# Performance work log

Measured on AMD Instinct MI355X. Metric: run time of the kernel, lower is better.

Reference implementation:

```python
import jax, jax.numpy as jnp
import numpy as np

B, NCH, NPTS, NGT = 8, 4, 1024, 10
NANCH = 5 * NPTS
NMIN, NMAX = 64, 64
M = NMIN + NMAX
NPOOL = 64
EXT = 0.2
EPS = 1e-5
PERM = np.array([3, 4, 5, 1, 0, 2, 6])

_C = jnp.array([[0., 1, 0], [0, -1, 0], [2.5, -1, 0], [2.5, 1, 0], [2.5, 0, 0]], jnp.float32)
_ROT = jnp.array([[1., 0, 0], [0, 0, 1], [0, 1, 0]], jnp.float32)  # theta=0 rotation from source
NEW_CENTERS = _C @ _ROT  # (5,3)
DIM = jnp.array([2., 2., 5.], jnp.float32)


def _conv1x1(x, w, b):
    return jnp.einsum('bci,oc->boi', x, w) + b[None, :, None]


def _bn(x, g, be):  # BatchNorm1d in train mode: batch stats over (N, L)
    m = x.mean((0, 2), keepdims=True)
    v = ((x - m) ** 2).mean((0, 2), keepdims=True)
    return (x - m) * jax.lax.rsqrt(v + EPS) * g[None, :, None] + be[None, :, None]


def _corners(b):  # b=(cx,cz,w,l,ry) -> (4,2) CCW BEV corners
    lx = jnp.array([0.5, -0.5, -0.5, 0.5]) * b[2]
    lz = jnp.array([0.5, 0.5, -0.5, -0.5]) * b[3]
    c, s = jnp.cos(b[4]), jnp.sin(b[4])
    return jnp.stack([b[0] + lx * c - lz * s, b[1] + lx * s + lz * c], 1)


def _clip(poly, count, e1, e2):  # Sutherland-Hodgman: clip convex poly (8,2) by left half-plane of e1->e2
    idx = jnp.arange(8)
    valid = idx < count
    cnt = jnp.maximum(count, 1)
    nxt = poly[(idx + 1) % cnt]
    ex, ez = e2[0] - e1[0], e2[1] - e1[1]
    dc = ex * (poly[:, 1] - e1[1]) - ez * (poly[:, 0] - e1[0])
    dn = ex * (nxt[:, 1] - e1[1]) - ez * (nxt[:, 0] - e1[0])
    in_c, in_n = dc >= 0, dn >= 0
    den = dc - dn
    t = dc / jnp.where(jnp.abs(den) < 1e-9, 1e-9, den)
    inter = poly + t[:, None] * (nxt - poly)
    flags = jnp.stack([valid & in_c, valid & (in_c ^ in_n)], 1).reshape(16)
    pts = jnp.stack([poly, inter], 1).reshape(16, 2)
    pos = jnp.cumsum(flags) - 1
    out = jnp.zeros((8, 2), poly.dtype).at[jnp.where(flags, pos, 8)].set(pts, mode='drop')
    return out, flags.sum()


def _bev_iou(a, b):  # rotated BEV IoU, a,b=(cx,cz,w,l,ry)
    poly = jnp.zeros((8, 2)).at[:4].set(_corners(a))
    count = jnp.int32(4)
    cb = _corners(b)
    for k in range(4):
        poly, count = _clip(poly, count, cb[k], cb[(k + 1) % 4])
    idx = jnp.arange(8)
    nxt = poly[(idx + 1) % jnp.maximum(count, 1)]
    inter = 0.5 * jnp.abs(jnp.sum(jnp.where(idx < count, poly[:, 0] * nxt[:, 1] - nxt[:, 0] * poly[:, 1], 0.)))
    return inter / jnp.maximum(a[2] * a[3] + b[2] * b[3] - inter, 1e-8)


def _bev(b7):  # (..,7)=[x,y,z,h,w,l,ry] -> (cx,cz,w,l,ry)
    return jnp.stack([b7[..., 0], b7[..., 2], b7[..., 4], b7[..., 5], b7[..., 6]], -1)


def _select_one(pnts, labels):  # pnts (N,3), labels (G,9)
    cent = (pnts[:, None, :] - NEW_CENTERS[None]).reshape(NANCH, 3)  # repeat_interleave(pnts,5)-tile(centers)
    anchors = jnp.concatenate([jnp.broadcast_to(DIM, (NANCH, 3)), cent, jnp.zeros((NANCH, 1))], 1)
    a7 = anchors[:, PERM]
    g7 = labels[:, PERM]
    ab, gb = _bev(a7), _bev(g7)
    iou2d = jax.vmap(lambda g: jax.vmap(lambda a: _bev_iou(g, a))(ab))(gb)  # (G, NANCH)
    max_iou = iou2d.max(0)
    max_ind = jnp.argmax(iou2d, 0)
    order = jnp.argsort(max_iou)
    sel = jnp.concatenate([order[:NMIN], order[-NMAX:]])  # bottom-k + top-k
    return a7[sel], max_ind[sel], max_iou[sel]


def _pool_one(box, pts, ft):  # roipool3d: first NPOOL points inside expanded box, zero-padded
    c, s = jnp.cos(box[6]), jnp.sin(box[6])
    dx, dz = pts[:, 0] - box[0], pts[:, 2] - box[2]
    xl = dx * c + dz * s
    zl = -dx * s + dz * c
    inside = (jnp.abs(xl) < box[4] * 0.5 + EXT) & (jnp.abs(zl) < box[5] * 0.5 + EXT) \
             & (pts[:, 1] > box[1] - box[3] - EXT) & (pts[:, 1] < box[1] + EXT)
    order = jnp.argsort(jnp.logical_not(inside))[:NPOOL]  # stable sort: inside points first, original order
    valid = inside[order].astype(ft.dtype)[:, None]
    return jnp.concatenate([ft[order], pts[order]], -1) * valid  # (NPOOL, 256+3)


def _forward(points, gt_labels, p):
    x = jax.nn.relu(_bn(_conv1x1(points, p['pn_w1'], p['pn_b1']), p['pn_g1'], p['pn_be1']))
    x = jax.nn.relu(_bn(_conv1x1(x, p['pn_w2'], p['pn_b2']), p['pn_g2'], p['pn_be2']))
    x = _bn(_conv1x1(x, p['pn_w3'], p['pn_b3']), p['pn_g3'], p['pn_be3'])  # (B,256,N)
    pts = jnp.transpose(points[:, :3, :], (0, 2, 1))  # (B,N,3)
    sel_boxes, sel_idx, sel_iou = jax.vmap(_select_one)(pts, gt_labels)  # (B,M,7),(B,M),(B,M)
    ftr = jnp.transpose(x, (0, 2, 1))  # (B,N,256)
    pooled = jax.vmap(lambda bx, pp, ff: jax.vmap(lambda b: _pool_one(b, pp, ff))(bx))(sel_boxes, pts, ftr)
    pooled = pooled - jnp.pad(sel_boxes[:, :, None, :3], ((0, 0), (0, 0), (0, 0), (256, 0)))  # subtract center from last 3 ch
    pf = jnp.transpose(pooled.reshape(B * M, NPOOL, 259), (0, 2, 1))  # (B*M,259,64)
    f = _bn(_conv1x1(pf, p['rp_w1'], p['rp_b1']), p['rp_g1'], p['rp_be1'])
    f = _bn(_conv1x1(f, p['rp_w2'], p['rp_b2']), p['rp_g2'], p['rp_be2'])
    feats = f.reshape(B, M, 1024, NPOOL).max(-1)
    labels_bin = (sel_iou > 0.5).astype(jnp.int32)
    return feats, labels_bin, sel_iou, sel_boxes, gt_labels[-1], sel_idx


def setup_inputs():
    key = jax.random.key(0)
    ks = jax.random.split(key, 16)
    points = jax.random.normal(ks[0], (B, NCH, NPTS), jnp.float32) * 3.0
    dims = jax.random.uniform(ks[1], (B, NGT, 3), minval=1.0, maxval=4.0)
    ctrs = jax.random.normal(ks[2], (B, NGT, 3)) * 3.0
    th = jax.random.uniform(ks[3], (B, NGT, 1), minval=-3.14, maxval=3.14)
    extra = jax.random.normal(ks[4], (B, NGT, 2))
    gt_labels = jnp.concatenate([dims, ctrs, th, extra], -1).astype(jnp.float32)  # (B,G,9)
    inp = {'points': points, 'gt_labels': gt_labels}
    shapes = [('pn', 1, 64, NCH), ('pn', 2, 128, 64), ('pn', 3, 256, 128), ('rp', 1, 512, 259), ('rp', 2, 1024, 512)]
    for j, (pre, n, o, i) in enumerate(shapes):
        inp[f'{pre}_w{n}'] = jax.random.normal(ks[5 + j], (o, i), jnp.float32) / np.sqrt(i).astype(np.float32)
        inp[f'{pre}_b{n}'] = jnp.zeros((o,), jnp.float32)
        inp[f'{pre}_g{n}'] = jnp.ones((o,), jnp.float32)
        inp[f'{pre}_be{n}'] = jnp.zeros((o,), jnp.float32)
    return inp


def reference(points, gt_labels, pn_w1, pn_b1, pn_g1, pn_be1, pn_w2, pn_b2, pn_g2, pn_be2, pn_w3, pn_b3, pn_g3, pn_be3, rp_w1, rp_b1, rp_g1, rp_be1, rp_w2, rp_b2, rp_g2, rp_be2):
    p = dict(pn_w1=pn_w1, pn_b1=pn_b1, pn_g1=pn_g1, pn_be1=pn_be1, pn_w2=pn_w2, pn_b2=pn_b2, pn_g2=pn_g2, pn_be2=pn_be2, pn_w3=pn_w3, pn_b3=pn_b3, pn_g3=pn_g3, pn_be3=pn_be3, rp_w1=rp_w1, rp_b1=rp_b1, rp_g1=rp_g1, rp_be1=rp_be1, rp_w2=rp_w2, rp_b2=rp_b2, rp_g2=rp_g2, rp_be2=rp_be2)
    return _forward(points, gt_labels, p)
```

## Files before the change

kernel.cpp:

```cpp
#include <hip/hip_runtime.h>
#include <hip/hip_bf16.h>
#include <float.h>
#include <math.h>


typedef __attribute__((ext_vector_type(8))) short short8;
typedef __attribute__((ext_vector_type(4))) float f32x4;

template <int CTRL>
__device__ __forceinline__ float dppmv(float x) {
  return __int_as_float(__builtin_amdgcn_update_dpp(
      0, __float_as_int(x), CTRL, 0xF, 0xF, true));
}
__device__ __forceinline__ float dpp_sum16(float x) {
  x += dppmv<0xB1>(x);
  x += dppmv<0x4E>(x);
  x += dppmv<0x124>(x);
  x += dppmv<0x128>(x);
  return x;
}

__device__ __forceinline__ void stage1k(const unsigned short* g, unsigned short* l) {
  __builtin_amdgcn_global_load_lds(
      (const __attribute__((address_space(1))) unsigned int*)g,
      (__attribute__((address_space(3))) unsigned int*)l, 16, 0, 0);
}

#define FMA16()                                                                 \
  do {                                                                          \
    float4 av = *(const float4*)&sWT[cc][to * 4];                               \
    float4 bv = *(const float4*)&sB[cc][tk * 4];                                \
    acc[0][0] = fmaf(av.x, bv.x, acc[0][0]);                                    \
    acc[0][1] = fmaf(av.x, bv.y, acc[0][1]);                                    \
    acc[0][2] = fmaf(av.x, bv.z, acc[0][2]);                                    \
    acc[0][3] = fmaf(av.x, bv.w, acc[0][3]);                                    \
    acc[1][0] = fmaf(av.y, bv.x, acc[1][0]);                                    \
    acc[1][1] = fmaf(av.y, bv.y, acc[1][1]);                                    \
    acc[1][2] = fmaf(av.y, bv.z, acc[1][2]);                                    \
    acc[1][3] = fmaf(av.y, bv.w, acc[1][3]);                                    \
    acc[2][0] = fmaf(av.z, bv.x, acc[2][0]);                                    \
    acc[2][1] = fmaf(av.z, bv.y, acc[2][1]);                                    \
    acc[2][2] = fmaf(av.z, bv.z, acc[2][2]);                                    \
    acc[2][3] = fmaf(av.z, bv.w, acc[2][3]);                                    \
    acc[3][0] = fmaf(av.w, bv.x, acc[3][0]);                                    \
    acc[3][1] = fmaf(av.w, bv.y, acc[3][1]);                                    \
    acc[3][2] = fmaf(av.w, bv.z, acc[3][2]);                                    \
    acc[3][3] = fmaf(av.w, bv.w, acc[3][3]);                                    \
  } while (0)

template <int C, int O, bool AFF, bool RELU, bool TRANS>
__global__ __launch_bounds__(256) void conv_pn(const float* __restrict__ in,
                                               const float* __restrict__ w,
                                               const float* __restrict__ bias,
                                               const float* __restrict__ aff,
                                               float* __restrict__ out) {
  __shared__ __align__(16) float sB[64][68];
  __shared__ __align__(16) float sWT[64][68];
  const int i0 = blockIdx.x * 64;
  const int o0 = blockIdx.y * 64;
  const int b = blockIdx.z;
  const int tid = threadIdx.x;
  const int tk = tid & 15, to = tid >> 4;
  float acc[4][4] = {};
  for (int c0 = 0; c0 < C; c0 += 64) {
    const int cs = (C - c0 < 64) ? (C - c0) : 64;
    for (int idx = tid; idx < 4096; idx += 256) {
      int ii = idx & 63, cc = idx >> 6;
      float v = 0.f;
      if (cc < cs) {
        int c = c0 + cc;
        v = in[(b * C + c) * 1024 + i0 + ii];
        if (AFF) v = fmaf(v, aff[c], aff[C + c]);
        if (RELU) v = fmaxf(v, 0.f);
      }
      sB[cc][ii] = v;
    }
    for (int idx = tid; idx < 4096; idx += 256) {
      int cc = idx & 63, oo = idx >> 6;
      sWT[cc][oo] = (cc < cs) ? w[(o0 + oo) * C + c0 + cc] : 0.f;
    }
    __syncthreads();
    for (int cc = 0; cc < cs; ++cc) { FMA16(); }
    __syncthreads();
  }
  if (TRANS) {
    float b0 = bias[o0 + to * 4], b1 = bias[o0 + to * 4 + 1];
    float b2 = bias[o0 + to * 4 + 2], b3 = bias[o0 + to * 4 + 3];
#pragma unroll
    for (int jj = 0; jj < 4; ++jj) {
      float4 v = make_float4(acc[0][jj] + b0, acc[1][jj] + b1, acc[2][jj] + b2, acc[3][jj] + b3);
      *(float4*)&out[((size_t)(b * 1024) + i0 + tk * 4 + jj) * O + o0 + to * 4] = v;
    }
  } else {
    for (int j = 0; j < 4; ++j) {
      int o = o0 + to * 4 + j;
      float bs = bias[o];
      float4 v = make_float4(acc[j][0] + bs, acc[j][1] + bs, acc[j][2] + bs, acc[j][3] + bs);
      *(float4*)&out[(b * O + o) * 1024 + i0 + tk * 4] = v;
    }
  }
}

__global__ __launch_bounds__(256) void bn_stats(const float* __restrict__ x,
                                                const float* __restrict__ g,
                                                const float* __restrict__ be,
                                                float* __restrict__ aff, int C) {
#pragma clang fp contract(off)
  int c = blockIdx.x;
  int tid = threadIdx.x;
  float s = 0.f, q = 0.f;
  for (int idx = tid; idx < 8192; idx += 256) {
    int b = idx >> 10, i = idx & 1023;
    float v = x[(b * C + c) * 1024 + i];
    s += v;
    q += v * v;
  }
  for (int m = 1; m < 64; m <<= 1) {
    s += __shfl_xor(s, m);
    q += __shfl_xor(q, m);
  }
  __shared__ float as_[4], aq_[4];
  int wv = tid >> 6;
  if ((tid & 63) == 0) { as_[wv] = s; aq_[wv] = q; }
  __syncthreads();
  if (tid == 0) {
    s = as_[0] + as_[1] + as_[2] + as_[3];
    q = aq_[0] + aq_[1] + aq_[2] + aq_[3];
    float m_ = s * (1.f / 8192.f);
    float var = q * (1.f / 8192.f) - m_ * m_;
    float A = g[c] / sqrtf(var + 1e-5f);
    aff[c] = A;
    aff[C + c] = be[c] - m_ * A;
  }
}

__device__ __forceinline__ void poly_ins(float* ox, float* oz, int p, float vx, float vz) {
#pragma unroll
  for (int s = 0; s < 8; ++s)
    if (p == s) { ox[s] = vx; oz[s] = vz; }
}

__device__ float bev_iou_ga(const float* gx, const float* gz, float garea, float ax, float az) {
#pragma clang fp contract(off)
  float px[8], pz[8];
#pragma unroll
  for (int i = 0; i < 4; ++i) {
    px[i] = gx[i];
    pz[i] = gz[i];
    px[i + 4] = 0.f;
    pz[i + 4] = 0.f;
  }
  int count = 4;
  float kx[4], kz[4];
  kx[0] = ax + 1.f;  kz[0] = az + 2.5f;
  kx[1] = ax - 1.f;  kz[1] = az + 2.5f;
  kx[2] = ax - 1.f;  kz[2] = az - 2.5f;
  kx[3] = ax + 1.f;  kz[3] = az - 2.5f;
#pragma unroll
  for (int e = 0; e < 4; ++e) {
    float e1x = kx[e], e1z = kz[e];
    float e2x = kx[(e + 1) & 3], e2z = kz[(e + 1) & 3];
    float ex = e2x - e1x, ez = e2z - e1z;
    int cnt = count > 1 ? count : 1;
    int lim = count < 8 ? count : 8;
    float ox[8] = {}, oz[8] = {};
    int p = 0;
#pragma unroll
    for (int idx = 0; idx < 8; ++idx) {
      if (idx < lim) {
        const int nis = (idx + 1 > 7) ? 7 : idx + 1;
        float nx = px[nis], nz = pz[nis];
        if (idx + 1 == cnt) { nx = px[0]; nz = pz[0]; }
        float cx = px[idx], cz = pz[idx];
        float dc = ex * (cz - e1z) - ez * (cx - e1x);
        float dn = ex * (nz - e1z) - ez * (nx - e1x);
        bool ic = dc >= 0.f, in_ = dn >= 0.f;
        if (ic) {
          poly_ins(ox, oz, p, cx, cz);
          ++p;
        }
        if (ic != in_) {
          float den = dc - dn;
          float t = dc / (fabsf(den) < 1e-9f ? 1e-9f : den);
          poly_ins(ox, oz, p, cx + t * (nx - cx), cz + t * (nz - cz));
          ++p;
        }
      }
    }
    count = p;
    int cp = p < 8 ? p : 8;
#pragma unroll
    for (int i = 0; i < 8; ++i) {
      px[i] = (i < cp) ? ox[i] : 0.f;
      pz[i] = (i < cp) ? oz[i] : 0.f;
    }
  }
  int cnt = count > 1 ? count : 1;
  int lim = count < 8 ? count : 8;
  float ssum = 0.f;
#pragma unroll
  for (int idx = 0; idx < 8; ++idx) {
    if (idx < lim) {
      const int nis = (idx + 1 > 7) ? 7 : idx + 1;
      float nx = px[nis], nz = pz[nis];
      if (idx + 1 == cnt) { nx = px[0]; nz = pz[0]; }
      ssum += px[idx] * nz - nx * pz[idx];
    }
  }
  float inter = 0.5f * fabsf(ssum);
  return inter / fmaxf(garea + 10.f - inter, 1e-8f);
}

__global__ __launch_bounds__(256) void fused_mid(
    const float* __restrict__ in2, const float* __restrict__ w3,
    const float* __restrict__ b3, const float* __restrict__ aff2,
    float* __restrict__ out3T,
    const float* __restrict__ points, const float* __restrict__ gt,
    float* __restrict__ iou10, float* __restrict__ o_gt, int* __restrict__ rank,
    const float* __restrict__ w1, unsigned short* __restrict__ W1f) {
  __shared__ __align__(16) float sB[64][68];
  __shared__ __align__(16) float sWT[64][68];
  const int bid = blockIdx.x;
  const int tid = threadIdx.x;
  if (bid < 512) {
    const int i0 = (bid & 15) * 64;
    const int o0 = ((bid >> 4) & 3) * 64;
    const int b = bid >> 6;
    const int tk = tid & 15, to = tid >> 4;
    float acc[4][4] = {};
    for (int c0 = 0; c0 < 128; c0 += 64) {
      for (int idx = tid; idx < 4096; idx += 256) {
        int ii = idx & 63, cc = idx >> 6;
        int c = c0 + cc;
        float v = in2[(b * 128 + c) * 1024 + i0 + ii];
        v = fmaf(v, aff2[c], aff2[128 + c]);
        v = fmaxf(v, 0.f);
        sB[cc][ii] = v;
      }
      for (int idx = tid; idx < 4096; idx += 256) {
        int cc = idx & 63, oo = idx >> 6;
        sWT[cc][oo] = w3[(o0 + oo) * 128 + c0 + cc];
      }
      __syncthreads();
      for (int cc = 0; cc < 64; ++cc) { FMA16(); }
      __syncthreads();
    }
    float c0v = b3[o0 + to * 4], c1v = b3[o0 + to * 4 + 1];
    float c2v = b3[o0 + to * 4 + 2], c3v = b3[o0 + to * 4 + 3];
#pragma unroll
    for (int jj = 0; jj < 4; ++jj) {
      float4 v = make_float4(acc[0][jj] + c0v, acc[1][jj] + c1v, acc[2][jj] + c2v, acc[3][jj] + c3v);
      *(float4*)&out3T[((size_t)(b * 1024) + i0 + tk * 4 + jj) * 256 + o0 + to * 4] = v;
    }
  } else if (bid < 2112) {
#pragma clang fp contract(off)
    int r = bid - 512;
    int g = r / 160;
    int rb = r % 160;
    int b = rb / 20;
    int axb = rb % 20;
    int a = axb * 256 + tid;
    if (g == 0) rank[b * 5120 + a] = 0;
    if (g == 0 && b == 0 && axb == 0 && tid < 90)
      o_gt[tid] = gt[630 + tid];
    const float* L = gt + b * 90 + g * 9;
    float gxx = L[3], gzz = L[5], gw = L[0], gl = L[2], gth = L[6];
    float c = cosf(gth), s = sinf(gth);
    const float sx[4] = {0.5f, -0.5f, -0.5f, 0.5f};
    const float sz[4] = {0.5f, 0.5f, -0.5f, -0.5f};
    float gcx[4], gcz[4];
#pragma unroll
    for (int k = 0; k < 4; ++k) {
      float lx = sx[k] * gw, lz = sz[k] * gl;
      gcx[k] = gxx + lx * c - lz * s;
      gcz[k] = gzz + lx * s + lz * c;
    }
    float garea = gw * gl;
    int pt = a / 5, j = a % 5;
    const float CX[5] = {0.f, 0.f, 2.5f, 2.5f, 2.5f};
    const float CZ[5] = {1.f, -1.f, -1.f, 1.f, 0.f};
    const float* P = points + b * 4096;
    float ax = P[pt] - CX[j];
    float az = P[2048 + pt] - CZ[j];
    iou10[(size_t)(b * 10 + g) * 5120 + a] = bev_iou_ga(gcx, gcz, garea, ax, az);
  } else {
    int o = (bid - 2112) * 4 + (tid >> 6);
    int lp = tid & 63;
    if (lp < 36) {
      int ks = lp >> 2, quad = lp & 3;
      int tile = o >> 4;
      union { __hip_bfloat16 h[8]; uint4 u; } pk;
#pragma unroll
      for (int j = 0; j < 8; ++j) {
        int c = ks * 32 + quad * 8 + j;
        float v = (c < 259) ? w1[o * 259 + c] : 0.f;
        pk.h[j] = __float2bfloat16(v);
      }
      *(uint4*)&W1f[((size_t)(tile * 9 + ks) * 64 + quad * 16 + (o & 15)) * 8] = pk.u;
    }
  }
}

__global__ __launch_bounds__(256) void bn_iou_red(
    const float* __restrict__ x, const float* __restrict__ g,
    const float* __restrict__ be, float* __restrict__ aff,
    const float* __restrict__ iou10, float* __restrict__ maxiou,
    int* __restrict__ maxind) {
  const int bid = blockIdx.x;
  const int tid = threadIdx.x;
  if (bid < 256) {
#pragma clang fp contract(off)
    int c = bid;
    float s = 0.f, q = 0.f;
    for (int idx = tid; idx < 8192; idx += 256) {
      float v = x[(size_t)idx * 256 + c];
      s += v;
      q += v * v;
    }
    for (int m = 1; m < 64; m <<= 1) {
      s += __shfl_xor(s, m);
      q += __shfl_xor(q, m);
    }
    __shared__ float as_[4], aq_[4];
    int wv = tid >> 6;
    if ((tid & 63) == 0) { as_[wv] = s; aq_[wv] = q; }
    __syncthreads();
    if (tid == 0) {
      s = as_[0] + as_[1] + as_[2] + as_[3];
      q = aq_[0] + aq_[1] + aq_[2] + aq_[3];
      float m_ = s * (1.f / 8192.f);
      float var = q * (1.f / 8192.f) - m_ * m_;
      float A = g[c] / sqrtf(var + 1e-5f);
      aff[c] = A;
      aff[256 + c] = be[c] - m_ * A;
    }
  } else {
    int r = bid - 256;
    int b = r / 20;
    int a = (r % 20) * 256 + tid;
    float best = -1.f;
    int bi = 0;
    for (int g2 = 0; g2 < 10; ++g2) {
      float v = iou10[(size_t)(b * 10 + g2) * 5120 + a];
      if (v > best) { best = v; bi = g2; }
    }
    maxiou[b * 5120 + a] = best;
    maxind[b * 5120 + a] = bi;
  }
}

__global__ __launch_bounds__(256) void select_rank(const float* __restrict__ maxiou,
                                                   int* __restrict__ rank) {
  __shared__ __align__(16) float vals[640];
  int b = blockIdx.y, chunk = blockIdx.z, tid = threadIdx.x;
  int jb0 = chunk * 640;
  for (int i = tid; i < 640; i += 256) vals[i] = maxiou[b * 5120 + jb0 + i];
  int a = blockIdx.x * 256 + tid;
  float av = maxiou[b * 5120 + a];
  __syncthreads();
  int rk = 0;
#pragma unroll 4
  for (int j4 = 0; j4 < 160; ++j4) {
    float4 v = *(const float4*)&vals[j4 * 4];
    int jb = jb0 + j4 * 4;
    rk += (v.x < av) || (v.x == av && jb < a);
    rk += (v.y < av) || (v.y == av && jb + 1 < a);
    rk += (v.z < av) || (v.z == av && jb + 2 < a);
    rk += (v.w < av) || (v.w == av && jb + 3 < a);
  }
  atomicAdd(&rank[b * 5120 + a], rk);
}

__global__ __launch_bounds__(256) void select_write(const int* __restrict__ rank,
                                                    const float* __restrict__ maxiou,
                                                    const int* __restrict__ maxind,
                                                    const float* __restrict__ points,
                                                    float* __restrict__ o_lbl,
                                                    float* __restrict__ o_iou,
                                                    float* __restrict__ o_box,
                                                    float* __restrict__ o_idx) {
#pragma clang fp contract(off)
  int b = blockIdx.y, tid = threadIdx.x;
  int a = blockIdx.x * 256 + tid;
  int rk = rank[b * 5120 + a];
  int slot = -1;
  if (rk < 64) slot = rk;
  else if (rk >= 5056) slot = rk - 4992;
  if (slot >= 0) {
    const float CX[5] = {0.f, 0.f, 2.5f, 2.5f, 2.5f};
    const float CZ[5] = {1.f, -1.f, -1.f, 1.f, 0.f};
    int base = b * 128 + slot;
    float av = maxiou[b * 5120 + a];
    o_iou[base] = av;
    o_lbl[base] = av > 0.5f ? 1.f : 0.f;
    o_idx[base] = (float)maxind[b * 5120 + a];
    int pt = a / 5, j = a % 5;
    const float* P = points + b * 4096;
    float* bx = o_box + base * 7;
    bx[0] = P[pt] - CX[j];
    bx[1] = P[1024 + pt];
    bx[2] = P[2048 + pt] - CZ[j];
    bx[3] = 2.f;
    bx[4] = 2.f;
    bx[5] = 5.f;
    bx[6] = 0.f;
  }
}

__global__ __launch_bounds__(256) void pool_kernel(const float* __restrict__ points,
                                                   const float* __restrict__ selboxes,
                                                   int* __restrict__ selpts) {
#pragma clang fp contract(off)
  int box = blockIdx.x * 4 + (threadIdx.x >> 6);
  int lane = threadIdx.x & 63;
  int b = box >> 7;
  const float* bx = selboxes + box * 7;
  float b0 = bx[0], b1 = bx[1], b2 = bx[2], b3 = bx[3], b4 = bx[4], b5 = bx[5];
  float limx = b4 * 0.5f + 0.2f, limz = b5 * 0.5f + 0.2f;
  float ylo = b1 - b3 - 0.2f, yhi = b1 + 0.2f;
  const float* P = points + b * 4096;
  unsigned long long m[16];
  int total_in = 0;
#pragma unroll
  for (int r = 0; r < 16; ++r) {
    int pt = r * 64 + lane;
    float dx = P[pt] - b0;
    float py = P[1024 + pt];
    float dz = P[2048 + pt] - b2;
    bool ins = (fabsf(dx) < limx) && (fabsf(dz) < limz) && (py > ylo) && (py < yhi);
    m[r] = __ballot(ins);
    total_in += __popcll(m[r]);
  }
  unsigned long long lowmask = (1ull << lane) - 1;
  int cum = 0;
#pragma unroll
  for (int r = 0; r < 16; ++r) {
    int pt = r * 64 + lane;
    int inbefore = cum + __popcll(m[r] & lowmask);
    bool ins = (m[r] >> lane) & 1;
    int slot = ins ? inbefore : total_in + (pt - inbefore);
    if (slot < 64) selpts[box * 64 + slot] = pt | (ins ? 0x10000 : 0);
    cum += __popcll(m[r]);
  }
}

__global__ __launch_bounds__(1024) void gather_rp1(
    const float* __restrict__ out3T, const float* __restrict__ points,
    const int* __restrict__ selpts, const float* __restrict__ selboxes,
    const float* __restrict__ aff3, const float* __restrict__ bias1,
    const unsigned short* __restrict__ W1f, unsigned short* __restrict__ g1x,
    float* __restrict__ psum4, float* __restrict__ psq4) {
  __shared__ __align__(16) unsigned short sBuf[18432];
  __shared__ int sSel[64];
  __shared__ float sCen[3];
  __shared__ float sA3[256], sB3[256];
  const int bm = blockIdx.x;
  const int b = bm >> 7;
  const int tid = threadIdx.x;
  if (tid < 64) sSel[tid] = selpts[bm * 64 + tid];
  if (tid >= 64 && tid < 67) sCen[tid - 64] = selboxes[bm * 7 + (tid - 64)];
  if (tid >= 256 && tid < 512) sA3[tid - 256] = aff3[tid - 256];
  if (tid >= 512 && tid < 768) sB3[tid - 512] = aff3[256 + tid - 512];
  __syncthreads();
  for (int u = tid; u < 2304; u += 1024) {
    int ks, pool, part;
    if (u < 2048) {
      ks = u >> 8;
      int rem = u & 255;
      pool = rem >> 2;
      part = rem & 3;
    } else {
      int v = u - 2048;
      ks = 8;
      pool = v >> 2;
      part = v & 3;
    }
    const int ni = pool >> 4, nib = pool & 15;
    const int sv = sSel[pool];
    const int pt = sv & 0xFFFF;
    const bool valid = (sv >> 16) != 0;
    union { __hip_bfloat16 h[8]; uint4 uu; } pk;
    if (ks < 8) {
      const float* row = out3T + ((size_t)(b << 10) + pt) * 256;
      int c0 = ks * 32 + part * 8;
      float4 x0 = *(const float4*)&row[c0];
      float4 x1 = *(const float4*)&row[c0 + 4];
      float v[8] = {x0.x, x0.y, x0.z, x0.w, x1.x, x1.y, x1.z, x1.w};
#pragma unroll
      for (int e = 0; e < 8; ++e) {
        float vv = valid ? fmaf(v[e], sA3[c0 + e], sB3[c0 + e]) : 0.f;
        pk.h[e] = __float2bfloat16(vv);
      }
    } else {
#pragma unroll
      for (int e = 0; e < 8; ++e) pk.h[e] = __float2bfloat16(0.f);
      if (part == 0) {
#pragma unroll
        for (int d = 0; d < 3; ++d) {
          float pv = valid ? points[(b * 4 + d) * 1024 + pt] : 0.f;
          pk.h[d] = __float2bfloat16(pv - sCen[d]);
        }
      }
    }
    *(uint4*)&sBuf[(size_t)(((ks * 4 + ni) * 64) + part * 16 + nib) * 8] = pk.uu;
  }
  __syncthreads();
  const int lane = tid & 63, wv = tid >> 6;
  const int ot = wv >> 2, w = wv & 3;
  const int quad = lane >> 4, nib = lane & 15;
  const unsigned short* Aw = &W1f[((size_t)(ot * 8 + w * 2) * 9 * 64 + lane) * 8];
  const unsigned short* Bl = &sBuf[lane * 8];
  f32x4 acc[2][4] = {};
#pragma unroll
  for (int ks = 0; ks < 9; ++ks) {
    short8 af[2], bf[4];
#pragma unroll
    for (int mi = 0; mi < 2; ++mi)
      af[mi] = *(const short8*)&Aw[(size_t)(mi * 9 + ks) * 512];
#pragma unroll
    for (int ni = 0; ni < 4; ++ni)
      bf[ni] = *(const short8*)&Bl[(size_t)(ks * 4 + ni) * 512];
#pragma unroll
    for (int mi = 0; mi < 2; ++mi)
#pragma unroll
      for (int ni = 0; ni < 4; ++ni)
        acc[mi][ni] = __builtin_amdgcn_mfma_f32_16x16x32_bf16(af[mi], bf[ni], acc[mi][ni], 0, 0, 0);
  }
  const int cbase = ot * 128 + w * 32;
#pragma unroll
  for (int mi = 0; mi < 2; ++mi) {
    float bv[4];
#pragma unroll
    for (int r = 0; r < 4; ++r) bv[r] = bias1[cbase + mi * 16 + quad * 4 + r];
    float s[4] = {0.f, 0.f, 0.f, 0.f}, q[4] = {0.f, 0.f, 0.f, 0.f};
    const int kgbase = (cbase + mi * 16) >> 3;
#pragma unroll
    for (int ni = 0; ni < 4; ++ni) {
      union { __hip_bfloat16 h[4]; unsigned int u[2]; } pk;
#pragma unroll
      for (int r = 0; r < 4; ++r) {
        float v = acc[mi][ni][r] + bv[r];
        pk.h[r] = __float2bfloat16(v);
        s[r] += v;
        q[r] += v * v;
      }
      unsigned int p0 = (unsigned int)__shfl_xor((int)pk.u[0], 16);
      unsigned int p1 = (unsigned int)__shfl_xor((int)pk.u[1], 16);
      if ((quad & 1) == 0) {
        uint4 g = make_uint4(pk.u[0], pk.u[1], p0, p1);
        int kg = kgbase + (quad >> 1);
        *(uint4*)&g1x[((size_t)(bm * 64 + kg) * 64 + ni * 16 + nib) * 8] = g;
      }
    }
#pragma unroll
    for (int r = 0; r < 4; ++r) {
      float ss = dpp_sum16(s[r]);
      float qq = dpp_sum16(q[r]);
      if (nib == 0) {
        int o = cbase + mi * 16 + quad * 4 + r;
        psum4[(size_t)o * 1024 + bm] = ss;
        psq4[(size_t)o * 1024 + bm] = qq;
      }
    }
  }
}

__global__ __launch_bounds__(64) void bn_aff_part(const float* __restrict__ psum,
                                                  const float* __restrict__ psq,
                                                  const float* __restrict__ g,
                                                  const float* __restrict__ be,
                                                  float* __restrict__ aff, int C) {
#pragma clang fp contract(off)
  int o = blockIdx.x;
  int lane = threadIdx.x;
  float s = 0.f, q = 0.f;
  for (int i = 0; i < 16; ++i) {
    int bm = i * 64 + lane;
    s += psum[(size_t)o * 1024 + bm];
    q += psq[(size_t)o * 1024 + bm];
  }
  for (int m = 1; m < 64; m <<= 1) {
    s += __shfl_xor(s, m);
    q += __shfl_xor(q, m);
  }
  if (lane == 0) {
    float m_ = s * (1.f / 65536.f);
    float var = q * (1.f / 65536.f) - m_ * m_;
    float A = g[o] / sqrtf(var + 1e-5f);
    aff[o] = A;
    aff[C + o] = be[o] - m_ * A;
  }
}

__global__ __launch_bounds__(64) void prep_w2(const float* __restrict__ w2,
                                              const float* __restrict__ b2,
                                              const float* __restrict__ aff4,
                                              unsigned short* __restrict__ W2f,
                                              float* __restrict__ bias2p) {
  int o = blockIdx.x;
  int lp = threadIdx.x;
  int ks = lp >> 2, quad = lp & 3;
  int tile = o >> 4;
  float accb = 0.f;
  union { __hip_bfloat16 h[8]; uint4 u; } pk;
#pragma unroll
  for (int j = 0; j < 8; ++j) {
    int c = ks * 32 + quad * 8 + j;
    float wv = w2[o * 512 + c];
    pk.h[j] = __float2bfloat16(wv * aff4[c]);
    accb += wv * aff4[512 + c];
  }
  *(uint4*)&W2f[((size_t)(tile * 16 + ks) * 64 + quad * 16 + (o & 15)) * 8] = pk.u;
  for (int m = 1; m < 64; m <<= 1) accb += __shfl_xor(accb, m);
  if (lp == 0) bias2p[o] = b2[o] + accb;
}

__global__ __launch_bounds__(256) void rp2_mfma(const unsigned short* __restrict__ W2f,
                                                const unsigned short* __restrict__ g1x,
                                                const float* __restrict__ bias2p,
                                                float* __restrict__ maxb,
                                                float* __restrict__ minb,
                                                float* __restrict__ psum,
                                                float* __restrict__ psq) {
  __shared__ __align__(16) unsigned short sBuf[2][8192];
  const int tid = threadIdx.x;
  const int lane = tid & 63, w = tid >> 6;
  const int quad = lane >> 4, nib = lane & 15;
  const int l = blockIdx.x;
  const int xcd = l & 7;
  const int j = l >> 3;
  const int ot = j & 3;
  const int bm = xcd * 128 + (j >> 2);
  const unsigned short* Aw = &W2f[((size_t)(ot * 4 + w) * 4 * 16 * 64 + lane) * 8];
  const unsigned short* Bg = g1x + (size_t)bm * 32768 + w * 2048 + lane * 8;
#pragma unroll
  for (int i = 0; i < 4; ++i)
    stage1k(Bg + i * 512, &sBuf[0][w * 2048 + i * 512]);
  __syncthreads();
  f32x4 acc[4][4] = {};
  int cur = 0;
#pragma unroll
  for (int c = 0; c < 4; ++c) {
    if (c < 3) {
#pragma unroll
      for (int i = 0; i < 4; ++i)
        stage1k(Bg + (c + 1) * 8192 + i * 512, &sBuf[cur ^ 1][w * 2048 + i * 512]);
    }
    const unsigned short* Bl = &sBuf[cur][quad * 512 + nib * 8];
#pragma unroll
    for (int k2 = 0; k2 < 4; ++k2) {
      const int ks = c * 4 + k2;
      short8 af[4], bf[4];
#pragma unroll
      for (int mi = 0; mi < 4; ++mi)
        af[mi] = *(const short8*)&Aw[(size_t)(mi * 16 + ks) * 512];
#pragma unroll
      for (int ni = 0; ni < 4; ++ni)
        bf[ni] = *(const short8*)&Bl[(size_t)(k2 * 2048 + ni * 128)];
#pragma unroll
      for (int mi = 0; mi < 4; ++mi)
#pragma unroll
        for (int ni = 0; ni < 4; ++ni)
          acc[ni][mi] = __builtin_amdgcn_mfma_f32_16x16x32_bf16(bf[ni], af[mi], acc[ni][mi], 0, 0, 0);
    }
    __syncthreads();
    cur ^= 1;
  }
  const int obase = ot * 256 + w * 64;
#pragma unroll
  for (int oi = 0; oi < 4; ++oi) {
    int o = obase + oi * 16 + nib;
    float bs = bias2p[o];
    float mx = -FLT_MAX, mn = FLT_MAX, s = 0.f, q = 0.f;
#pragma unroll
    for (int pi = 0; pi < 4; ++pi) {
#pragma unroll
      for (int r = 0; r < 4; ++r) {
        float v = acc[pi][oi][r] + bs;
        mx = fmaxf(mx, v);
        mn = fminf(mn, v);
        s += v;
        q += v * v;
      }
    }
    mx = fmaxf(mx, __shfl_xor(mx, 16));
    mx = fmaxf(mx, __shfl_xor(mx, 32));
    mn = fminf(mn, __shfl_xor(mn, 16));
    mn = fminf(mn, __shfl_xor(mn, 32));
    s += __shfl_xor(s, 16);
    s += __shfl_xor(s, 32);
    q += __shfl_xor(q, 16);
    q += __shfl_xor(q, 32);
    if (quad == 0) {
      maxb[bm * 1024 + o] = mx;
      minb[bm * 1024 + o] = mn;
      psum[(size_t)o * 1024 + bm] = s;
      psq[(size_t)o * 1024 + bm] = q;
    }
  }
}

__global__ void feats_kernel(const float* __restrict__ maxb, const float* __restrict__ minb,
                             const float* __restrict__ aff5, float* __restrict__ o_feats) {
#pragma clang fp contract(off)
  int i = blockIdx.x * 256 + threadIdx.x;
  int o = i & 1023;
  float A = aff5[o], Bv = aff5[1024 + o];
  float v = (A >= 0.f) ? maxb[i] : minb[i];
  o_feats[i] = v * A + Bv;
}

extern "C" void kernel_launch(void* const* d_in, const int* in_sizes, int n_in,
                              void* d_out, int out_size, void* d_ws, size_t ws_size,
                              hipStream_t stream) {
  (void)in_sizes; (void)n_in; (void)out_size; (void)ws_size;
  const float* points = (const float*)d_in[0];
  const float* gt = (const float*)d_in[1];
  const float* pn_w1 = (const float*)d_in[2];
  const float* pn_b1 = (const float*)d_in[3];
  const float* pn_g1 = (const float*)d_in[4];
  const float* pn_be1 = (const float*)d_in[5];
  const float* pn_w2 = (const float*)d_in[6];
  const float* pn_b2 = (const float*)d_in[7];
  const float* pn_g2 = (const float*)d_in[8];
  const float* pn_be2 = (const float*)d_in[9];
  const float* pn_w3 = (const float*)d_in[10];
  const float* pn_b3 = (const float*)d_in[11];
  const float* pn_g3 = (const float*)d_in[12];
  const float* pn_be3 = (const float*)d_in[13];
  const float* rp_w1 = (const float*)d_in[14];
  const float* rp_b1 = (const float*)d_in[15];
  const float* rp_g1 = (const float*)d_in[16];
  const float* rp_be1 = (const float*)d_in[17];
  const float* rp_w2 = (const float*)d_in[18];
  const float* rp_b2 = (const float*)d_in[19];
  const float* rp_g2 = (const float*)d_in[20];
  const float* rp_be2 = (const float*)d_in[21];

  float* ws = (float*)d_ws;
  float* out1 = ws;
  float* out2 = out1 + 524288;
  float* maxiou = out2 + 1048576;
  int* maxind = (int*)(maxiou + 40960);
  int* selpts = maxind + 40960;
  int* rank = selpts + 65536;
  float* aff1 = (float*)(rank + 40960);
  float* aff2 = aff1 + 128;
  float* aff3 = aff2 + 256;
  float* aff4 = aff3 + 512;
  float* aff5 = aff4 + 1024;
  float* psum4 = aff5 + 2048;
  float* psq4 = psum4 + 524288;
  unsigned short* W1f = (unsigned short*)(psq4 + 524288);
  float* pff_f = (float*)(W1f) + 73728;
  float* out3T = pff_f;
  float* maxb = pff_f + 2097152;
  float* minb = maxb + 1048576;
  float* psum5 = minb + 1048576;
  float* psq5 = psum5 + 1048576;
  float* g1x_f = pff_f + 9437184;
  unsigned short* g1x = (unsigned short*)g1x_f;
  float* iou10 = g1x_f + 2097152;
  unsigned short* W2f = (unsigned short*)out1;
  float* bias2p = out1 + 262144;

  float* o_feats = (float*)d_out;
  float* o_lbl = o_feats + 1048576;
  float* o_iou = o_lbl + 1024;
  float* o_box = o_iou + 1024;
  float* o_gt = o_box + 7168;
  float* o_idx = o_gt + 90;

  conv_pn<4, 64, false, false, false><<<dim3(16, 1, 8), 256, 0, stream>>>(points, pn_w1, pn_b1, nullptr, out1);
  bn_stats<<<64, 256, 0, stream>>>(out1, pn_g1, pn_be1, aff1, 64);
  conv_pn<64, 128, true, true, false><<<dim3(16, 2, 8), 256, 0, stream>>>(out1, pn_w2, pn_b2, aff1, out2);
  bn_stats<<<128, 256, 0, stream>>>(out2, pn_g2, pn_be2, aff2, 128);
  fused_mid<<<2240, 256, 0, stream>>>(out2, pn_w3, pn_b3, aff2, out3T,
                                      points, gt, iou10, o_gt, rank,
                                      rp_w1, W1f);
  bn_iou_red<<<416, 256, 0, stream>>>(out3T, pn_g3, pn_be3, aff3,
                                      iou10, maxiou, maxind);
  select_rank<<<dim3(20, 8, 8), 256, 0, stream>>>(maxiou, rank);
  select_write<<<dim3(20, 8), 256, 0, stream>>>(rank, maxiou, maxind, points, o_lbl, o_iou, o_box, o_idx);
  pool_kernel<<<256, 256, 0, stream>>>(points, o_box, selpts);
  gather_rp1<<<1024, 1024, 0, stream>>>(out3T, points, selpts, o_box, aff3,
                                        rp_b1, W1f, g1x, psum4, psq4);
  bn_aff_part<<<512, 64, 0, stream>>>(psum4, psq4, rp_g1, rp_be1, aff4, 512);
  prep_w2<<<1024, 64, 0, stream>>>(rp_w2, rp_b2, aff4, W2f, bias2p);
  rp2_mfma<<<4096, 256, 0, stream>>>(W2f, g1x, bias2p, maxb, minb, psum5, psq5);
  bn_aff_part<<<1024, 64, 0, stream>>>(psum5, psq5, rp_g2, rp_be2, aff5, 1024);
  feats_kernel<<<4096, 256, 0, stream>>>(maxb, minb, aff5, o_feats);
}
```

Before: 344.5 us.

## Fuse rank selection kernels and fold point pooling into gather_rp1

Merges select_rank and select_write into one rank_write kernel. Each block now loads all 5120 max-IoU values into shared memory and computes the full rank itself, with no atomics and no rank-zeroing in fused_mid. The separate pool_kernel is removed, and gather_rp1 computes each box's in-box point selection with a block-wide ballot and prefix count. This cuts two kernel launches and the global round trips for rank and selpts. In exchange, the rank kernel runs 160 blocks each doing an 8x longer serial loop instead of 1280 shorter blocks.

```diff
diff --git a/kernel.cpp b/kernel.cpp
--- a/kernel.cpp
+++ b/kernel.cpp
@@ -216,7 +216,7 @@
     const float* __restrict__ b3, const float* __restrict__ aff2,
     float* __restrict__ out3T,
     const float* __restrict__ points, const float* __restrict__ gt,
-    float* __restrict__ iou10, float* __restrict__ o_gt, int* __restrict__ rank,
+    float* __restrict__ iou10, float* __restrict__ o_gt,
     const float* __restrict__ w1, unsigned short* __restrict__ W1f) {
   __shared__ __align__(16) float sB[64][68];
   __shared__ __align__(16) float sWT[64][68];
@@ -260,7 +260,6 @@
     int b = rb / 20;
     int axb = rb % 20;
     int a = axb * 256 + tid;
-    if (g == 0) rank[b * 5120 + a] = 0;
     if (g == 0 && b == 0 && axb == 0 && tid < 90)
       o_gt[tid] = gt[630 + tid];
     const float* L = gt + b * 90 + g * 9;
@@ -349,40 +348,29 @@
   }
 }
 
-__global__ __launch_bounds__(256) void select_rank(const float* __restrict__ maxiou,
-                                                   int* __restrict__ rank) {
-  __shared__ __align__(16) float vals[640];
-  int b = blockIdx.y, chunk = blockIdx.z, tid = threadIdx.x;
-  int jb0 = chunk * 640;
-  for (int i = tid; i < 640; i += 256) vals[i] = maxiou[b * 5120 + jb0 + i];
-  int a = blockIdx.x * 256 + tid;
+__global__ __launch_bounds__(256) void rank_write(
+    const float* __restrict__ maxiou, const int* __restrict__ maxind,
+    const float* __restrict__ points,
+    float* __restrict__ o_lbl, float* __restrict__ o_iou,
+    float* __restrict__ o_box, float* __restrict__ o_idx) {
+#pragma clang fp contract(off)
+  __shared__ __align__(16) float vals[5120];
+  const int b = blockIdx.y;
+  const int tid = threadIdx.x;
+  const int a = blockIdx.x * 256 + tid;
+  for (int i = tid; i < 5120; i += 256) vals[i] = maxiou[b * 5120 + i];
   float av = maxiou[b * 5120 + a];
   __syncthreads();
   int rk = 0;
 #pragma unroll 4
-  for (int j4 = 0; j4 < 160; ++j4) {
+  for (int j4 = 0; j4 < 1280; ++j4) {
     float4 v = *(const float4*)&vals[j4 * 4];
-    int jb = jb0 + j4 * 4;
+    int jb = j4 * 4;
     rk += (v.x < av) || (v.x == av && jb < a);
     rk += (v.y < av) || (v.y == av && jb + 1 < a);
     rk += (v.z < av) || (v.z == av && jb + 2 < a);
     rk += (v.w < av) || (v.w == av && jb + 3 < a);
   }
-  atomicAdd(&rank[b * 5120 + a], rk);
-}
-
-__global__ __launch_bounds__(256) void select_write(const int* __restrict__ rank,
-                                                    const float* __restrict__ maxiou,
-                                                    const int* __restrict__ maxind,
-                                                    const float* __restrict__ points,
-                                                    float* __restrict__ o_lbl,
-                                                    float* __restrict__ o_iou,
-                                                    float* __restrict__ o_box,
-                                                    float* __restrict__ o_idx) {
-#pragma clang fp contract(off)
-  int b = blockIdx.y, tid = threadIdx.x;
-  int a = blockIdx.x * 256 + tid;
-  int rk = rank[b * 5120 + a];
   int slot = -1;
   if (rk < 64) slot = rk;
   else if (rk >= 5056) slot = rk - 4992;
@@ -390,7 +378,6 @@
     const float CX[5] = {0.f, 0.f, 2.5f, 2.5f, 2.5f};
     const float CZ[5] = {1.f, -1.f, -1.f, 1.f, 0.f};
     int base = b * 128 + slot;
-    float av = maxiou[b * 5120 + a];
     o_iou[base] = av;
     o_lbl[base] = av > 0.5f ? 1.f : 0.f;
     o_idx[base] = (float)maxind[b * 5120 + a];
@@ -407,61 +394,54 @@
   }
 }
 
-__global__ __launch_bounds__(256) void pool_kernel(const float* __restrict__ points,
-                                                   const float* __restrict__ selboxes,
-                                                   int* __restrict__ selpts) {
+__device__ __forceinline__ bool pool_inside(const float* __restrict__ P,
+                                            const float* bx, int pt) {
 #pragma clang fp contract(off)
-  int box = blockIdx.x * 4 + (threadIdx.x >> 6);
-  int lane = threadIdx.x & 63;
-  int b = box >> 7;
-  const float* bx = selboxes + box * 7;
-  float b0 = bx[0], b1 = bx[1], b2 = bx[2], b3 = bx[3], b4 = bx[4], b5 = bx[5];
-  float limx = b4 * 0.5f + 0.2f, limz = b5 * 0.5f + 0.2f;
-  float ylo = b1 - b3 - 0.2f, yhi = b1 + 0.2f;
-  const float* P = points + b * 4096;
-  unsigned long long m[16];
-  int total_in = 0;
-#pragma unroll
-  for (int r = 0; r < 16; ++r) {
-    int pt = r * 64 + lane;
-    float dx = P[pt] - b0;
-    float py = P[1024 + pt];
-    float dz = P[2048 + pt] - b2;
-    bool ins = (fabsf(dx) < limx) && (fabsf(dz) < limz) && (py > ylo) && (py < yhi);
-    m[r] = __ballot(ins);
-    total_in += __popcll(m[r]);
-  }
-  unsigned long long lowmask = (1ull << lane) - 1;
-  int cum = 0;
-#pragma unroll
-  for (int r = 0; r < 16; ++r) {
-    int pt = r * 64 + lane;
-    int inbefore = cum + __popcll(m[r] & lowmask);
-    bool ins = (m[r] >> lane) & 1;
-    int slot = ins ? inbefore : total_in + (pt - inbefore);
-    if (slot < 64) selpts[box * 64 + slot] = pt | (ins ? 0x10000 : 0);
-    cum += __popcll(m[r]);
-  }
+  float limx = bx[4] * 0.5f + 0.2f, limz = bx[5] * 0.5f + 0.2f;
+  float ylo = bx[1] - bx[3] - 0.2f, yhi = bx[1] + 0.2f;
+  float dx = P[pt] - bx[0];
+  float py = P[1024 + pt];
+  float dz = P[2048 + pt] - bx[2];
+  return (fabsf(dx) < limx) && (fabsf(dz) < limz) && (py > ylo) && (py < yhi);
 }
 
 __global__ __launch_bounds__(1024) void gather_rp1(
     const float* __restrict__ out3T, const float* __restrict__ points,
-    const int* __restrict__ selpts, const float* __restrict__ selboxes,
-    const float* __restrict__ aff3, const float* __restrict__ bias1,
-    const unsigned short* __restrict__ W1f, unsigned short* __restrict__ g1x,
+    const float* __restrict__ selboxes, const float* __restrict__ aff3,
+    const float* __restrict__ bias1, const unsigned short* __restrict__ W1f,
+    unsigned short* __restrict__ g1x,
     float* __restrict__ psum4, float* __restrict__ psq4) {
   __shared__ __align__(16) unsigned short sBuf[18432];
   __shared__ int sSel[64];
-  __shared__ float sCen[3];
+  __shared__ float sBox[8];
   __shared__ float sA3[256], sB3[256];
+  __shared__ int wcnt[16];
   const int bm = blockIdx.x;
   const int b = bm >> 7;
   const int tid = threadIdx.x;
-  if (tid < 64) sSel[tid] = selpts[bm * 64 + tid];
-  if (tid >= 64 && tid < 67) sCen[tid - 64] = selboxes[bm * 7 + (tid - 64)];
+  if (tid < 7) sBox[tid] = selboxes[bm * 7 + tid];
   if (tid >= 256 && tid < 512) sA3[tid - 256] = aff3[tid - 256];
   if (tid >= 512 && tid < 768) sB3[tid - 512] = aff3[256 + tid - 512];
   __syncthreads();
+  {
+    const float* P = points + b * 4096;
+    const int lane = tid & 63, w16 = tid >> 6;
+    bool ins = pool_inside(P, sBox, tid);
+    unsigned long long mw = __ballot(ins);
+    if (lane == 0) wcnt[w16] = __popcll(mw);
+    __syncthreads();
+    int cumw = 0, total = 0;
+#pragma unroll
+    for (int i = 0; i < 16; ++i) {
+      int c = wcnt[i];
+      total += c;
+      if (i < w16) cumw += c;
+    }
+    int inbefore = cumw + __popcll(mw & ((1ull << lane) - 1));
+    int slot = ins ? inbefore : total + (tid - inbefore);
+    if (slot < 64) sSel[slot] = tid | (ins ? 0x10000 : 0);
+    __syncthreads();
+  }
   for (int u = tid; u < 2304; u += 1024) {
     int ks, pool, part;
     if (u < 2048) {
@@ -498,7 +478,7 @@
 #pragma unroll
         for (int d = 0; d < 3; ++d) {
           float pv = valid ? points[(b * 4 + d) * 1024 + pt] : 0.f;
-          pk.h[d] = __float2bfloat16(pv - sCen[d]);
+          pk.h[d] = __float2bfloat16(pv - sBox[d]);
         }
       }
     }
@@ -776,14 +756,13 @@
   conv_pn<64, 128, true, true, false><<<dim3(16, 2, 8), 256, 0, stream>>>(out1, pn_w2, pn_b2, aff1, out2);
   bn_stats<<<128, 256, 0, stream>>>(out2, pn_g2, pn_be2, aff2, 128);
   fused_mid<<<2240, 256, 0, stream>>>(out2, pn_w3, pn_b3, aff2, out3T,
-                                      points, gt, iou10, o_gt, rank,
+                                      points, gt, iou10, o_gt,
                                       rp_w1, W1f);
   bn_iou_red<<<416, 256, 0, stream>>>(out3T, pn_g3, pn_be3, aff3,
                                       iou10, maxiou, maxind);
-  select_rank<<<dim3(20, 8, 8), 256, 0, stream>>>(maxiou, rank);
-  select_write<<<dim3(20, 8), 256, 0, stream>>>(rank, maxiou, maxind, points, o_lbl, o_iou, o_box, o_idx);
-  pool_kernel<<<256, 256, 0, stream>>>(points, o_box, selpts);
-  gather_rp1<<<1024, 1024, 0, stream>>>(out3T, points, selpts, o_box, aff3,
+  rank_write<<<dim3(20, 8), 256, 0, stream>>>(maxiou, maxind, points,
+                                              o_lbl, o_iou, o_box, o_idx);
+  gather_rp1<<<1024, 1024, 0, stream>>>(out3T, points, o_box, aff3,
                                         rp_b1, W1f, g1x, psum4, psq4);
   bn_aff_part<<<512, 64, 0, stream>>>(psum4, psq4, rp_g1, rp_be1, aff4, 512);
   prep_w2<<<1024, 64, 0, stream>>>(rp_w2, rp_b2, aff4, W2f, bias2p);
```

New measurement: 430.1 us. 1.25x slower.
